# Kernel tuning notes

Hardware: AMD Instinct MI355X
Metric: run time of the kernel (lower is better)

Reference implementation:

```python
import jax, jax.numpy as jnp
import numpy as np

B, S, E, H = 4, 2048, 1024, 16
HD = E // H  # head_dim = 64


def setup_inputs() -> dict:
    key = jax.random.key(0)
    k1, k2, k3, k4 = jax.random.split(key, 4)
    x = jax.random.normal(k1, (B, S, E), dtype=jnp.float32)
    Wqkv = jax.random.normal(k2, (3 * E, E), dtype=jnp.float32) * (E ** -0.5)
    Wo = jax.random.normal(k3, (E, E), dtype=jnp.float32) * (E ** -0.5)
    bo = jax.random.normal(k4, (E,), dtype=jnp.float32) * 0.01
    return {"x": x, "Wqkv": Wqkv, "Wo": Wo, "bo": bo}


def reference(x, Wqkv, Wo, bo):
    b, s, e = x.shape
    # qkv projection (nn.Linear without bias: x @ W^T) -> (b, s, 3e)
    qkv = x @ Wqkv.T
    # reshape (b, s, H, 3*HD) -> (b, H, s, 3*HD), then chunk into q,k,v
    qkv = qkv.reshape(b, s, H, 3 * HD).transpose(0, 2, 1, 3)
    q, k, v = jnp.split(qkv, 3, axis=-1)  # each (b, H, s, HD)
    scale = 1.0 / jnp.sqrt(jnp.asarray(HD, dtype=x.dtype))
    scores = jnp.einsum('bhqd,bhkd->bhqk', q, k) * scale  # (b, H, s, s)
    causal = jnp.tril(jnp.ones((s, s), dtype=bool))
    scores = jnp.where(causal, scores, -jnp.inf)
    probs = jax.nn.softmax(scores, axis=-1)
    out = jnp.einsum('bhqk,bhkd->bhqd', probs, v)  # (b, H, s, HD)
    out = out.transpose(0, 2, 1, 3).reshape(b, s, e)
    return out @ Wo.T + bo
```

## Files before the change

kernel.cpp:

```cpp
#include <hip/hip_runtime.h>
#include <stdint.h>

#define Bn 4
#define Sn 2048
#define En 1024
#define Hn 16
#define HDn 64

typedef __bf16 bf16;
typedef __bf16 bf16x4 __attribute__((ext_vector_type(4)));
typedef __bf16 bf16x8 __attribute__((ext_vector_type(8)));
typedef float  f32x4  __attribute__((ext_vector_type(4)));
typedef float  f32x16 __attribute__((ext_vector_type(16)));
typedef uint32_t u32x4 __attribute__((ext_vector_type(4)));

#define GLDS(gp, lp) __builtin_amdgcn_global_load_lds( \
    (const __attribute__((address_space(1))) void*)(gp), \
    (__attribute__((address_space(3))) void*)(lp), 16, 0, 0)

#define BAR() __builtin_amdgcn_s_barrier()
#define WLG() do { asm volatile("s_waitcnt lgkmcnt(0)" ::: "memory"); \
                   __builtin_amdgcn_sched_barrier(0); } while (0)
#define WVM4() asm volatile("s_waitcnt vmcnt(4)" ::: "memory")
#define WVM0() asm volatile("s_waitcnt vmcnt(0)" ::: "memory")

__global__ __launch_bounds__(256) void cvt_f32_to_bf16(
    const float* __restrict__ in, bf16* __restrict__ out, int n4)
{
    int i = blockIdx.x * 256 + threadIdx.x;
    if (i >= n4) return;
    float4 f = reinterpret_cast<const float4*>(in)[i];
    bf16x4 o;
    o[0] = (bf16)f.x; o[1] = (bf16)f.y; o[2] = (bf16)f.z; o[3] = (bf16)f.w;
    reinterpret_cast<bf16x4*>(out)[i] = o;
}

template<int MODE>
__global__ __launch_bounds__(512, 2) void gemm256(
    const bf16* __restrict__ Ag, const bf16* __restrict__ Bw,
    int M, int N, int K,
    bf16* __restrict__ q_out, bf16* __restrict__ k_out, bf16* __restrict__ v_out,
    float* __restrict__ c_out, const float* __restrict__ bias)
{
    __shared__ __align__(16) bf16 lA[2 * 256 * 64];
    __shared__ __align__(16) bf16 lB[2 * 256 * 64];

    const int tid  = threadIdx.x;
    const int lane = tid & 63;
    const int w    = tid >> 6;
    const int wm = w >> 2, wn = w & 3;
    const int lr = lane & 15, lg = lane >> 4;
    const int m0 = blockIdx.y * 256;
    const int n0 = blockIdx.x * 256;
    const int NT = K >> 6;
    const int niter = NT >> 1;

    const int srow = tid >> 3;
    const int sck  = (tid & 7) ^ ((tid >> 3) & 7);

    f32x4 acc[8][4] = {};

    auto stageA = [&](int t, int half) {
        const int ts = t < NT ? t : NT - 1;
        bf16* Ld = lA + ((t & 1) ? 16384 : 0) + (half*128 + w*8) * 64;
        const bf16* S = Ag + (size_t)(m0 + half*128 + srow) * K + ts*64 + sck*8;
        GLDS(S, Ld);
        GLDS(S + (size_t)64 * K, Ld + 64 * 64);
    };
    auto stageB = [&](int t, int half) {
        const int ts = t < NT ? t : NT - 1;
        bf16* Ld = lB + ((t & 1) ? 16384 : 0) + (half*128 + w*8) * 64;
        const bf16* S = Bw + (size_t)(n0 + half*128 + srow) * K + ts*64 + sck*8;
        GLDS(S, Ld);
        GLDS(S + (size_t)64 * K, Ld + 64 * 64);
    };
    auto ldA4 = [&](bf16x8 (&a)[4][2], const bf16* Lb, int qm) {
        #pragma unroll
        for (int ii = 0; ii < 4; ++ii) {
            const bf16* p = Lb + (wm*128 + qm*64 + ii*16 + lr) * 64;
            #pragma unroll
            for (int kk = 0; kk < 2; ++kk)
                a[ii][kk] = *reinterpret_cast<const bf16x8*>(p + (((kk << 2) + lg) ^ (lr & 7)) * 8);
        }
    };
    auto ldB2 = [&](bf16x8 (&b)[2][2], const bf16* Lb, int qn) {
        #pragma unroll
        for (int j = 0; j < 2; ++j) {
            const bf16* p = Lb + (wn*64 + qn*32 + j*16 + lr) * 64;
            #pragma unroll
            for (int kk = 0; kk < 2; ++kk)
                b[j][kk] = *reinterpret_cast<const bf16x8*>(p + (((kk << 2) + lg) ^ (lr & 7)) * 8);
        }
    };
    auto mmac = [&](const bf16x8 (&a)[4][2], const bf16x8 (&b)[2][2], int qm, int qn) {
        __builtin_amdgcn_s_setprio(1);
        #pragma unroll
        for (int ii = 0; ii < 4; ++ii)
            #pragma unroll
            for (int j = 0; j < 2; ++j)
                #pragma unroll
                for (int kk = 0; kk < 2; ++kk)
                    acc[qm*4 + ii][qn*2 + j] = __builtin_amdgcn_mfma_f32_16x16x32_bf16(
                        a[ii][kk], b[j][kk], acc[qm*4 + ii][qn*2 + j], 0, 0, 0);
        __builtin_amdgcn_s_setprio(0);
    };

    stageA(0, 0); stageA(0, 1); stageB(0, 0); stageB(0, 1);
    stageB(1, 0); stageB(1, 1);
    WVM4(); BAR();

    const bf16* A0 = lA;          const bf16* A1 = lA + 16384;
    const bf16* B0l = lB;         const bf16* B1l = lB + 16384;
    bf16x8 a[4][2], b0[2][2], b1[2][2];

    for (int i = 0; i < niter; ++i) {
        const int t = 2 * i;
        ldA4(a, A0, 0); ldB2(b0, B0l, 0);
        stageA(t + 1, 0);
        BAR(); WLG();
        mmac(a, b0, 0, 0);
        BAR();
        ldB2(b1, B0l, 1);
        stageA(t + 1, 1);
        BAR(); WLG();
        mmac(a, b1, 0, 1);
        BAR();
        ldA4(a, A0, 1);
        stageB(t + 2, 0);
        BAR(); WLG();
        mmac(a, b0, 1, 0);
        BAR();
        stageB(t + 2, 1);
        WVM4(); BAR();
        mmac(a, b1, 1, 1);
        BAR();
        ldA4(a, A1, 0); ldB2(b0, B1l, 0);
        stageA(t + 2, 0);
        BAR(); WLG();
        mmac(a, b0, 0, 0);
        BAR();
        ldB2(b1, B1l, 1);
        stageA(t + 2, 1);
        BAR(); WLG();
        mmac(a, b1, 0, 1);
        BAR();
        ldA4(a, A1, 1);
        stageB(t + 3, 0);
        BAR(); WLG();
        mmac(a, b0, 1, 0);
        BAR();
        stageB(t + 3, 1);
        WVM4(); BAR();
        mmac(a, b1, 1, 1);
        BAR();
    }

    #pragma unroll
    for (int ii = 0; ii < 8; ++ii) {
        #pragma unroll
        for (int j = 0; j < 4; ++j) {
            const int colb = n0 + wn*64 + j*16 + lr;
            #pragma unroll
            for (int r = 0; r < 4; ++r) {
                const int rowb = m0 + wm*128 + ii*16 + lg*4 + r;
                const float v = acc[ii][j][r];
                if (MODE == 0) {
                    const int bb = rowb >> 11, s = rowb & (Sn - 1);
                    const int h = colb / 192, rr = colb - h*192;
                    const int wq = rr >> 6, hd = rr & 63;
                    const size_t off = (((size_t)(bb*Hn + h))*Sn + s)*HDn + hd;
                    const bf16 bv = (bf16)v;
                    if (wq == 0)      q_out[off] = bv;
                    else if (wq == 1) k_out[off] = bv;
                    else              v_out[off] = bv;
                } else {
                    c_out[(size_t)rowb*N + colb] = v + bias[colb];
                }
            }
        }
    }
}

template<int MODE>
__global__ __launch_bounds__(256) void gemm_bt(
    const bf16* __restrict__ A, const bf16* __restrict__ Bw,
    int M, int N, int K,
    float* __restrict__ c_out, const float* __restrict__ bias)
{
    __shared__ bf16 lA[128*64];
    __shared__ bf16 lB[128*64];
    const int tid  = threadIdx.x;
    const int lane = tid & 63;
    const int wv   = tid >> 6;
    const int wm = wv >> 1, wn = wv & 1;
    const int m0 = blockIdx.y * 128;
    const int n0 = blockIdx.x * 128;
    const int lr = lane & 15, lg = lane >> 4;

    f32x4 acc[4][4] = {};

    const int rowA = wv*8 + (lane>>3);
    const int col8 = (lane&7)*8;

    for (int k0 = 0; k0 < K; k0 += 64) {
        #pragma unroll
        for (int c = 0; c < 4; ++c) {
            int row = c*32 + rowA;
            GLDS(A  + (size_t)(m0+row)*K + k0 + col8, lA + (c*32 + wv*8)*64);
            GLDS(Bw + (size_t)(n0+row)*K + k0 + col8, lB + (c*32 + wv*8)*64);
        }
        __syncthreads();
        #pragma unroll
        for (int kk = 0; kk < 64; kk += 32) {
            bf16x8 af[4], bfv[4];
            #pragma unroll
            for (int i = 0; i < 4; ++i)
                af[i] = *reinterpret_cast<const bf16x8*>(lA + (wm*64 + i*16 + lr)*64 + kk + lg*8);
            #pragma unroll
            for (int j = 0; j < 4; ++j)
                bfv[j] = *reinterpret_cast<const bf16x8*>(lB + (wn*64 + j*16 + lr)*64 + kk + lg*8);
            #pragma unroll
            for (int i = 0; i < 4; ++i)
                #pragma unroll
                for (int j = 0; j < 4; ++j)
                    acc[i][j] = __builtin_amdgcn_mfma_f32_16x16x32_bf16(af[i], bfv[j], acc[i][j], 0, 0, 0);
        }
        __syncthreads();
    }

    #pragma unroll
    for (int i = 0; i < 4; ++i) {
        #pragma unroll
        for (int j = 0; j < 4; ++j) {
            const int colb = n0 + wn*64 + j*16 + lr;
            #pragma unroll
            for (int r = 0; r < 4; ++r) {
                const int rowb = m0 + wm*64 + i*16 + lg*4 + r;
                c_out[(size_t)rowb*N + colb] = acc[i][j][r] + bias[colb];
            }
        }
    }
}

static __device__ __forceinline__ uint32_t pkbf(float lo, float hi)
{
    uint16_t a = __builtin_bit_cast(uint16_t, (bf16)lo);
    uint16_t b = __builtin_bit_cast(uint16_t, (bf16)hi);
    return (uint32_t)a | ((uint32_t)b << 16);
}

__global__ __launch_bounds__(512) void attn_fwd(
    const bf16* __restrict__ Q, const bf16* __restrict__ Kg, const bf16* __restrict__ Vg,
    bf16* __restrict__ O)
{
    __shared__ __align__(16) bf16 Kl[2][64*64];
    __shared__ __align__(16) bf16 Vt[2][64*64];

    const int tid  = threadIdx.x;
    const int lane = tid & 63;
    const int w    = tid >> 6;
    const int col  = lane & 31;
    const int hv   = lane >> 5;
    const int bh   = blockIdx.x;
    const int qb   = (gridDim.y - 1) - blockIdx.y;
    const int q0w  = qb*256 + w*32;
    const int qg   = q0w + col;

    const bf16* Qb = Q  + (size_t)bh*Sn*HDn;
    const bf16* Kb = Kg + (size_t)bh*Sn*HDn;
    const bf16* Vb = Vg + (size_t)bh*Sn*HDn;

    bf16x8 aq[4];
    #pragma unroll
    for (int ks = 0; ks < 4; ++ks)
        aq[ks] = *reinterpret_cast<const bf16x8*>(Qb + (size_t)qg*HDn + ks*16 + hv*8);

    f32x16 ov[2] = {};
    const float S2 = 0.18033688011112042f;
    float m_run = -1e30f, l_run = 0.f;

    const int srow = tid >> 3;
    const int scc  = tid & 7;
    const int koff = srow*64 + (scc ^ (srow & 7))*8;

    auto vWrite = [&](bf16* Vd, bf16x8 vv) {
        #pragma unroll
        for (int j = 0; j < 8; ++j) {
            const int chunk = (scc*8 + j)*8 + ((srow>>3) ^ scc);
            Vd[chunk*8 + (srow&7)] = vv[j];
        }
    };

    const int nkt = 4*(qb+1);

    {
        bf16x8 k0r = *reinterpret_cast<const bf16x8*>(Kb + (size_t)srow*HDn + scc*8);
        bf16x8 v0r = *reinterpret_cast<const bf16x8*>(Vb + (size_t)srow*HDn + scc*8);
        *reinterpret_cast<bf16x8*>(&Kl[0][koff]) = k0r;
        vWrite(&Vt[0][0], v0r);
    }
    __syncthreads();

    for (int kt = 0; kt < nkt; ++kt) {
        const int cur  = kt & 1;
        const int k0   = kt*64;
        const bool more = (kt + 1 < nkt);
        const bool skip = (k0 > q0w + 31);
        const int kn   = more ? (k0 + 64) : k0;

        bf16x8 kreg = *reinterpret_cast<const bf16x8*>(Kb + (size_t)(kn + srow)*HDn + scc*8);
        bf16x8 vreg = *reinterpret_cast<const bf16x8*>(Vb + (size_t)(kn + srow)*HDn + scc*8);

        if (!skip) {
            f32x16 st[2] = {};
            __builtin_amdgcn_s_setprio(1);
            #pragma unroll
            for (int kb = 0; kb < 2; ++kb) {
                const int key = kb*32 + col;
                #pragma unroll
                for (int ks = 0; ks < 4; ++ks) {
                    const int slot = (ks*2 + hv) ^ (key & 7);
                    bf16x8 kf = *reinterpret_cast<const bf16x8*>(&Kl[cur][0] + key*64 + slot*8);
                    st[kb] = __builtin_amdgcn_mfma_f32_32x32x16_bf16(kf, aq[ks], st[kb], 0, 0, 0);
                }
            }
            __builtin_amdgcn_s_setprio(0);

            if (k0 + 63 > q0w) {
                #pragma unroll
                for (int kb = 0; kb < 2; ++kb)
                    #pragma unroll
                    for (int r = 0; r < 16; ++r) {
                        const int keyg = k0 + kb*32 + (r&3) + 8*(r>>2) + 4*hv;
                        if (keyg > qg) st[kb][r] = -1e30f;
                    }
            }

            float m16[8];
            #pragma unroll
            for (int r = 0; r < 8; ++r)
                m16[r] = fmaxf(fmaxf(st[0][r], st[0][r+8]), fmaxf(st[1][r], st[1][r+8]));
            #pragma unroll
            for (int d = 4; d; d >>= 1)
                #pragma unroll
                for (int r = 0; r < d; ++r)
                    m16[r] = fmaxf(m16[r], m16[r+d]);
            float mx = fmaxf(m16[0], __shfl_xor(m16[0], 32));
            const float smax2 = mx * S2;

            if (!__all(smax2 - m_run <= 8.0f)) {
                const float mn = fmaxf(m_run, smax2);
                const float fr = exp2f(m_run - mn);
                l_run *= fr;
                #pragma unroll
                for (int hb = 0; hb < 2; ++hb)
                    #pragma unroll
                    for (int r = 0; r < 16; ++r)
                        ov[hb][r] *= fr;
                m_run = mn;
            }

            uint32_t wpk[2][8];
            float lsum = 0.f;
            #pragma unroll
            for (int kb = 0; kb < 2; ++kb) {
                float pr[8];
                #pragma unroll
                for (int i = 0; i < 8; ++i) {
                    const float e0 = exp2f(fmaf(st[kb][2*i],   S2, -m_run));
                    const float e1 = exp2f(fmaf(st[kb][2*i+1], S2, -m_run));
                    pr[i] = e0 + e1;
                    wpk[kb][i] = pkbf(e0, e1);
                }
                pr[0] += pr[4]; pr[1] += pr[5]; pr[2] += pr[6]; pr[3] += pr[7];
                pr[0] += pr[2]; pr[1] += pr[3];
                lsum += pr[0] + pr[1];
            }
            l_run += lsum;

            #pragma unroll
            for (int s = 0; s < 4; ++s) {
                const int kb = s >> 1, ls = s & 1;
                const uint32_t send0 = hv ? wpk[kb][4*ls+0] : wpk[kb][4*ls+2];
                const uint32_t send1 = hv ? wpk[kb][4*ls+1] : wpk[kb][4*ls+3];
                const uint32_t keep0 = hv ? wpk[kb][4*ls+2] : wpk[kb][4*ls+0];
                const uint32_t keep1 = hv ? wpk[kb][4*ls+3] : wpk[kb][4*ls+1];
                const uint32_t r0 = (uint32_t)__shfl_xor((int)send0, 32);
                const uint32_t r1 = (uint32_t)__shfl_xor((int)send1, 32);
                u32x4 pwv = { hv ? r0 : keep0, hv ? r1 : keep1,
                              hv ? keep0 : r0, hv ? keep1 : r1 };
                bf16x8 pB = __builtin_bit_cast(bf16x8, pwv);
                __builtin_amdgcn_s_setprio(1);
                #pragma unroll
                for (int hb = 0; hb < 2; ++hb) {
                    const int hd = hb*32 + col;
                    const int slot = (s*2 + hv) ^ ((hd>>3) & 7);
                    bf16x8 vf = *reinterpret_cast<const bf16x8*>(&Vt[cur][0] + hd*64 + slot*8);
                    ov[hb] = __builtin_amdgcn_mfma_f32_32x32x16_bf16(vf, pB, ov[hb], 0, 0, 0);
                }
                __builtin_amdgcn_s_setprio(0);
            }
        }

        WVM0();
        if (more) {
            *reinterpret_cast<bf16x8*>(&Kl[cur^1][koff]) = kreg;
            vWrite(&Vt[cur^1][0], vreg);
        }
        __syncthreads();
    }

    const float lt  = l_run + __shfl_xor(l_run, 32);
    const float inv = 1.0f / lt;
    const int b = bh >> 4, hh = bh & 15;
    bf16* Ob = O + ((size_t)(b*Sn + qg))*En + hh*HDn;
    #pragma unroll
    for (int hb = 0; hb < 2; ++hb)
        #pragma unroll
        for (int g = 0; g < 4; ++g) {
            bf16x4 o4;
            #pragma unroll
            for (int r4 = 0; r4 < 4; ++r4)
                o4[r4] = (bf16)(ov[hb][g*4 + r4] * inv);
            *reinterpret_cast<bf16x4*>(Ob + hb*32 + g*8 + 4*hv) = o4;
        }
}

extern "C" void kernel_launch(void* const* d_in, const int* in_sizes, int n_in,
                              void* d_out, int out_size, void* d_ws, size_t ws_size,
                              hipStream_t stream)
{
    (void)in_sizes; (void)n_in; (void)out_size; (void)ws_size;
    const float* x    = (const float*)d_in[0];
    const float* Wqkv = (const float*)d_in[1];
    const float* Wo   = (const float*)d_in[2];
    const float* bo   = (const float*)d_in[3];
    float* out = (float*)d_out;

    const size_t nBS = (size_t)Bn*Sn;
    char* ws = (char*)d_ws;
    bf16* xb    = (bf16*)ws; ws += nBS*En*2;
    bf16* wqkvb = (bf16*)ws; ws += (size_t)3*En*En*2;
    bf16* wob   = (bf16*)ws; ws += (size_t)En*En*2;
    bf16* Qb    = (bf16*)ws; ws += nBS*En*2;
    bf16* Kb    = (bf16*)ws; ws += nBS*En*2;
    bf16* Vb    = (bf16*)ws; ws += nBS*En*2;
    bf16* AO    = (bf16*)ws; ws += nBS*En*2;

    int n4 = (int)(nBS*En/4);
    cvt_f32_to_bf16<<<(n4+255)/256, 256, 0, stream>>>(x, xb, n4);
    n4 = 3*En*En/4;
    cvt_f32_to_bf16<<<(n4+255)/256, 256, 0, stream>>>(Wqkv, wqkvb, n4);
    n4 = En*En/4;
    cvt_f32_to_bf16<<<(n4+255)/256, 256, 0, stream>>>(Wo, wob, n4);

    gemm256<0><<<dim3(3*En/256, nBS/256), 512, 0, stream>>>(
        xb, wqkvb, (int)nBS, 3*En, En, Qb, Kb, Vb, nullptr, nullptr);

    attn_fwd<<<dim3(Bn*Hn, Sn/256), 512, 0, stream>>>(Qb, Kb, Vb, AO);

    gemm_bt<1><<<dim3(En/128, nBS/128), 256, 0, stream>>>(
        AO, wob, (int)nBS, En, En, out, bo);
}
```

Before: 202.4 us.

## Single-buffer attention K/V tiles with direct-to-LDS loads and permlane32 swap

The attention kernel drops its register-staged double buffer for K/V. Each iteration now does a barrier, loads K straight into LDS with global_load_lds and transposes V into LDS, then barriers again. The P-fragment exchange uses permlane32_swap instead of two shfl_xor plus selects, and the setprio hints are removed. This lowers register and LDS pressure and the cost of the exchange, but gives up overlapping the next tile's global loads with the current tile's compute, so load latency is exposed every iteration.

New measurement: 196.0 us. -3.2%, faster.

```diff
diff --git a/kernel.cpp b/kernel.cpp
--- a/kernel.cpp
+++ b/kernel.cpp
@@ -13,6 +13,7 @@
 typedef float  f32x4  __attribute__((ext_vector_type(4)));
 typedef float  f32x16 __attribute__((ext_vector_type(16)));
 typedef uint32_t u32x4 __attribute__((ext_vector_type(4)));
+typedef int      i32x2 __attribute__((ext_vector_type(2)));
 
 #define GLDS(gp, lp) __builtin_amdgcn_global_load_lds( \
     (const __attribute__((address_space(1))) void*)(gp), \
@@ -22,7 +23,11 @@
 #define WLG() do { asm volatile("s_waitcnt lgkmcnt(0)" ::: "memory"); \
                    __builtin_amdgcn_sched_barrier(0); } while (0)
 #define WVM4() asm volatile("s_waitcnt vmcnt(4)" ::: "memory")
-#define WVM0() asm volatile("s_waitcnt vmcnt(0)" ::: "memory")
+
+static __device__ __forceinline__ i32x2 plsw(uint32_t a, uint32_t b)
+{
+    return __builtin_amdgcn_permlane32_swap((int)a, (int)b, false, false);
+}
 
 __global__ __launch_bounds__(256) void cvt_f32_to_bf16(
     const float* __restrict__ in, bf16* __restrict__ out, int n4)
@@ -181,7 +186,6 @@
     }
 }
 
-template<int MODE>
 __global__ __launch_bounds__(256) void gemm_bt(
     const bf16* __restrict__ A, const bf16* __restrict__ Bw,
     int M, int N, int K,
@@ -253,8 +257,8 @@
     const bf16* __restrict__ Q, const bf16* __restrict__ Kg, const bf16* __restrict__ Vg,
     bf16* __restrict__ O)
 {
-    __shared__ __align__(16) bf16 Kl[2][64*64];
-    __shared__ __align__(16) bf16 Vt[2][64*64];
+    __shared__ __align__(16) bf16 Kl[64*64];
+    __shared__ __align__(16) bf16 Vt[64*64];
 
     const int tid  = threadIdx.x;
     const int lane = tid & 63;
@@ -279,135 +283,112 @@
     const float S2 = 0.18033688011112042f;
     float m_run = -1e30f, l_run = 0.f;
 
-    const int srow = tid >> 3;
+    const int skey = tid >> 3;
     const int scc  = tid & 7;
-    const int koff = srow*64 + (scc ^ (srow & 7))*8;
-
-    auto vWrite = [&](bf16* Vd, bf16x8 vv) {
-        #pragma unroll
-        for (int j = 0; j < 8; ++j) {
-            const int chunk = (scc*8 + j)*8 + ((srow>>3) ^ scc);
-            Vd[chunk*8 + (srow&7)] = vv[j];
-        }
-    };
+    const int ksw  = scc ^ (skey & 7);
 
     const int nkt = 4*(qb+1);
-
-    {
-        bf16x8 k0r = *reinterpret_cast<const bf16x8*>(Kb + (size_t)srow*HDn + scc*8);
-        bf16x8 v0r = *reinterpret_cast<const bf16x8*>(Vb + (size_t)srow*HDn + scc*8);
-        *reinterpret_cast<bf16x8*>(&Kl[0][koff]) = k0r;
-        vWrite(&Vt[0][0], v0r);
-    }
-    __syncthreads();
-
     for (int kt = 0; kt < nkt; ++kt) {
-        const int cur  = kt & 1;
-        const int k0   = kt*64;
-        const bool more = (kt + 1 < nkt);
-        const bool skip = (k0 > q0w + 31);
-        const int kn   = more ? (k0 + 64) : k0;
-
-        bf16x8 kreg = *reinterpret_cast<const bf16x8*>(Kb + (size_t)(kn + srow)*HDn + scc*8);
-        bf16x8 vreg = *reinterpret_cast<const bf16x8*>(Vb + (size_t)(kn + srow)*HDn + scc*8);
-
-        if (!skip) {
-            f32x16 st[2] = {};
-            __builtin_amdgcn_s_setprio(1);
-            #pragma unroll
-            for (int kb = 0; kb < 2; ++kb) {
-                const int key = kb*32 + col;
+        const int k0 = kt*64;
+        __syncthreads();
+        GLDS(Kb + (size_t)(k0 + skey)*HDn + ksw*8, Kl + (size_t)w*512);
+        {
+            bf16x8 vv = *reinterpret_cast<const bf16x8*>(Vb + (size_t)(k0 + skey)*HDn + scc*8);
+            #pragma unroll
+            for (int j = 0; j < 8; ++j) {
+                const int chunk = (scc*8 + j)*8 + ((skey>>3) ^ scc);
+                Vt[chunk*8 + (skey&7)] = vv[j];
+            }
+        }
+        __syncthreads();
+
+        if (k0 > q0w + 31) continue;
+
+        f32x16 st[2] = {};
+        #pragma unroll
+        for (int kb = 0; kb < 2; ++kb) {
+            const int key = kb*32 + col;
+            #pragma unroll
+            for (int ks = 0; ks < 4; ++ks) {
+                const int chunk = key*8 + ((ks*2 + hv) ^ (key & 7));
+                bf16x8 kf = *reinterpret_cast<const bf16x8*>(Kl + chunk*8);
+                st[kb] = __builtin_amdgcn_mfma_f32_32x32x16_bf16(kf, aq[ks], st[kb], 0, 0, 0);
+            }
+        }
+
+        if (k0 + 63 > q0w) {
+            #pragma unroll
+            for (int kb = 0; kb < 2; ++kb)
                 #pragma unroll
-                for (int ks = 0; ks < 4; ++ks) {
-                    const int slot = (ks*2 + hv) ^ (key & 7);
-                    bf16x8 kf = *reinterpret_cast<const bf16x8*>(&Kl[cur][0] + key*64 + slot*8);
-                    st[kb] = __builtin_amdgcn_mfma_f32_32x32x16_bf16(kf, aq[ks], st[kb], 0, 0, 0);
+                for (int r = 0; r < 16; ++r) {
+                    const int keyg = k0 + kb*32 + (r&3) + 8*(r>>2) + 4*hv;
+                    if (keyg > qg) st[kb][r] = -1e30f;
                 }
-            }
-            __builtin_amdgcn_s_setprio(0);
-
-            if (k0 + 63 > q0w) {
+        }
+
+        float m16[8];
+        #pragma unroll
+        for (int r = 0; r < 8; ++r)
+            m16[r] = fmaxf(fmaxf(st[0][r], st[0][r+8]), fmaxf(st[1][r], st[1][r+8]));
+        #pragma unroll
+        for (int d = 4; d; d >>= 1)
+            #pragma unroll
+            for (int r = 0; r < d; ++r)
+                m16[r] = fmaxf(m16[r], m16[r+d]);
+        float mx = fmaxf(m16[0], __shfl_xor(m16[0], 32));
+        const float smax2 = mx * S2;
+
+        if (!__all(smax2 - m_run <= 8.0f)) {
+            const float mn = fmaxf(m_run, smax2);
+            const float fr = exp2f(m_run - mn);
+            l_run *= fr;
+            #pragma unroll
+            for (int hb = 0; hb < 2; ++hb)
                 #pragma unroll
-                for (int kb = 0; kb < 2; ++kb)
-                    #pragma unroll
-                    for (int r = 0; r < 16; ++r) {
-                        const int keyg = k0 + kb*32 + (r&3) + 8*(r>>2) + 4*hv;
-                        if (keyg > qg) st[kb][r] = -1e30f;
-                    }
-            }
-
-            float m16[8];
-            #pragma unroll
-            for (int r = 0; r < 8; ++r)
-                m16[r] = fmaxf(fmaxf(st[0][r], st[0][r+8]), fmaxf(st[1][r], st[1][r+8]));
-            #pragma unroll
-            for (int d = 4; d; d >>= 1)
-                #pragma unroll
-                for (int r = 0; r < d; ++r)
-                    m16[r] = fmaxf(m16[r], m16[r+d]);
-            float mx = fmaxf(m16[0], __shfl_xor(m16[0], 32));
-            const float smax2 = mx * S2;
-
-            if (!__all(smax2 - m_run <= 8.0f)) {
-                const float mn = fmaxf(m_run, smax2);
-                const float fr = exp2f(m_run - mn);
-                l_run *= fr;
-                #pragma unroll
-                for (int hb = 0; hb < 2; ++hb)
-                    #pragma unroll
-                    for (int r = 0; r < 16; ++r)
-                        ov[hb][r] *= fr;
-                m_run = mn;
-            }
-
-            uint32_t wpk[2][8];
-            float lsum = 0.f;
-            #pragma unroll
-            for (int kb = 0; kb < 2; ++kb) {
-                float pr[8];
-                #pragma unroll
-                for (int i = 0; i < 8; ++i) {
-                    const float e0 = exp2f(fmaf(st[kb][2*i],   S2, -m_run));
-                    const float e1 = exp2f(fmaf(st[kb][2*i+1], S2, -m_run));
-                    pr[i] = e0 + e1;
-                    wpk[kb][i] = pkbf(e0, e1);
-                }
-                pr[0] += pr[4]; pr[1] += pr[5]; pr[2] += pr[6]; pr[3] += pr[7];
-                pr[0] += pr[2]; pr[1] += pr[3];
-                lsum += pr[0] + pr[1];
-            }
-            l_run += lsum;
-
-            #pragma unroll
-            for (int s = 0; s < 4; ++s) {
-                const int kb = s >> 1, ls = s & 1;
-                const uint32_t send0 = hv ? wpk[kb][4*ls+0] : wpk[kb][4*ls+2];
-                const uint32_t send1 = hv ? wpk[kb][4*ls+1] : wpk[kb][4*ls+3];
-                const uint32_t keep0 = hv ? wpk[kb][4*ls+2] : wpk[kb][4*ls+0];
-                const uint32_t keep1 = hv ? wpk[kb][4*ls+3] : wpk[kb][4*ls+1];
-                const uint32_t r0 = (uint32_t)__shfl_xor((int)send0, 32);
-                const uint32_t r1 = (uint32_t)__shfl_xor((int)send1, 32);
-                u32x4 pwv = { hv ? r0 : keep0, hv ? r1 : keep1,
-                              hv ? keep0 : r0, hv ? keep1 : r1 };
-                bf16x8 pB = __builtin_bit_cast(bf16x8, pwv);
-                __builtin_amdgcn_s_setprio(1);
-                #pragma unroll
-                for (int hb = 0; hb < 2; ++hb) {
-                    const int hd = hb*32 + col;
-                    const int slot = (s*2 + hv) ^ ((hd>>3) & 7);
-                    bf16x8 vf = *reinterpret_cast<const bf16x8*>(&Vt[cur][0] + hd*64 + slot*8);
-                    ov[hb] = __builtin_amdgcn_mfma_f32_32x32x16_bf16(vf, pB, ov[hb], 0, 0, 0);
-                }
-                __builtin_amdgcn_s_setprio(0);
-            }
-        }
-
-        WVM0();
-        if (more) {
-            *reinterpret_cast<bf16x8*>(&Kl[cur^1][koff]) = kreg;
-            vWrite(&Vt[cur^1][0], vreg);
-        }
-        __syncthreads();
+                for (int r = 0; r < 16; ++r)
+                    ov[hb][r] *= fr;
+            m_run = mn;
+        }
+
+        uint32_t wpk[2][8];
+        float lsum = 0.f;
+        #pragma unroll
+        for (int kb = 0; kb < 2; ++kb) {
+            float pr[8];
+            #pragma unroll
+            for (int i = 0; i < 8; ++i) {
+                const float e0 = exp2f(fmaf(st[kb][2*i],   S2, -m_run));
+                const float e1 = exp2f(fmaf(st[kb][2*i+1], S2, -m_run));
+                pr[i] = e0 + e1;
+                wpk[kb][i] = pkbf(e0, e1);
+            }
+            pr[0] += pr[4]; pr[1] += pr[5]; pr[2] += pr[6]; pr[3] += pr[7];
+            pr[0] += pr[2]; pr[1] += pr[3];
+            lsum += pr[0] + pr[1];
+        }
+        l_run += lsum;
+
+        bf16x8 pB[4];
+        #pragma unroll
+        for (int s = 0; s < 4; ++s) {
+            const int kb = s >> 1, ls = s & 1;
+            i32x2 r02 = plsw(wpk[kb][4*ls+0], wpk[kb][4*ls+2]);
+            i32x2 r13 = plsw(wpk[kb][4*ls+1], wpk[kb][4*ls+3]);
+            u32x4 pwv = { (uint32_t)r02[0], (uint32_t)r13[0],
+                          (uint32_t)r02[1], (uint32_t)r13[1] };
+            pB[s] = __builtin_bit_cast(bf16x8, pwv);
+        }
+
+        #pragma unroll
+        for (int s = 0; s < 4; ++s) {
+            #pragma unroll
+            for (int hb = 0; hb < 2; ++hb) {
+                const int hd = hb*32 + col;
+                const int chunk = hd*8 + ((s*2 + hv) ^ ((hd>>3) & 7));
+                bf16x8 vf = *reinterpret_cast<const bf16x8*>(Vt + chunk*8);
+                ov[hb] = __builtin_amdgcn_mfma_f32_32x32x16_bf16(vf, pB[s], ov[hb], 0, 0, 0);
+            }
+        }
     }
 
     const float lt  = l_run + __shfl_xor(l_run, 32);
@@ -459,6 +440,6 @@
 
     attn_fwd<<<dim3(Bn*Hn, Sn/256), 512, 0, stream>>>(Qb, Kb, Vb, AO);
 
-    gemm_bt<1><<<dim3(En/128, nBS/128), 256, 0, stream>>>(
+    gemm_bt<<<dim3(En/128, nBS/128), 256, 0, stream>>>(
         AO, wob, (int)nBS, En, En, out, bo);
 }
```
